# Kernel optimization log

Measured on AMD Instinct MI355X. Metric: run time of the kernel, lower is better.

The kernel has to match this reference:

```python
import jax, jax.numpy as jnp
import numpy as np

DIM = 1024
HEADS = 16
HEAD_DIM = DIM // HEADS


def setup_inputs() -> dict:
    key = jax.random.key(0)
    ks = jax.random.split(key, 9)
    s = 1.0 / np.sqrt(DIM)
    return {
        "x": jax.random.normal(ks[0], (2, 2048, 1, DIM), dtype=jnp.float32),
        "Wq": jax.random.normal(ks[1], (DIM, DIM), dtype=jnp.float32) * s,
        "bq": jnp.zeros((DIM,), dtype=jnp.float32),
        "Wk": jax.random.normal(ks[2], (DIM, DIM), dtype=jnp.float32) * s,
        "bk": jnp.zeros((DIM,), dtype=jnp.float32),
        "Wv": jax.random.normal(ks[3], (DIM, DIM), dtype=jnp.float32) * s,
        "bv": jnp.zeros((DIM,), dtype=jnp.float32),
        "Wo": jax.random.normal(ks[4], (DIM, DIM), dtype=jnp.float32) * s,
        "bo": jnp.zeros((DIM,), dtype=jnp.float32),
    }


def reference(x, Wq, bq, Wk, bk, Wv, bv, Wo, bo):
    b, t, _, d = x.shape
    h, hd = HEADS, HEAD_DIM
    # torch Linear: y = x @ W.T + b
    q = (x @ Wq.T + bq).reshape(b, t, h, hd)
    k = (x @ Wk.T + bk).reshape(b, t, h, hd)
    v = (x @ Wv.T + bv).reshape(b, t, h, hd)
    # Source applies self.scaling (hd**-0.5) in torch AND divides by
    # sqrt(k_features) inside the jax chunk routine -> net scale 1/hd.
    q = q * (1.0 / hd)
    # key_chunk_size >= T -> one chunk; online softmax == exact stable softmax
    scores = jnp.einsum('bqhd,bkhd->bhqk', q, k)  # [B,H,T,T]
    w = jax.nn.softmax(scores, axis=-1)
    o = jnp.einsum('bhqk,bkhd->bqhd', w, v).reshape(b, t, d)
    return o @ Wo.T + bo
```

## Files before the change

### kernel.cpp

```cpp
#include <hip/hip_runtime.h>
#include <math.h>

typedef _Float16 f16;
typedef _Float16 f16x2 __attribute__((ext_vector_type(2)));
typedef _Float16 f16x4 __attribute__((ext_vector_type(4)));
typedef _Float16 f16x8 __attribute__((ext_vector_type(8)));
typedef float    f32x4 __attribute__((ext_vector_type(4)));

constexpr int DIM   = 1024;
constexpr int HEADS = 16;
constexpr int HD    = 64;
constexpr int BATCH = 2;
constexpr int SEQ   = 2048;
constexpr int MTOT  = BATCH * SEQ;
constexpr int NT2   = SEQ / 128;

#define QSCALE (1.4426950408889634f / 64.0f)

#define MFMA16(a, b, c) __builtin_amdgcn_mfma_f32_16x16x32_f16((a), (b), (c), 0, 0, 0)

__device__ __forceinline__ void glds16(const void* g, void* l) {
    __builtin_amdgcn_global_load_lds(
        (const __attribute__((address_space(1))) void*)g,
        (__attribute__((address_space(3))) void*)l, 16, 0, 0);
}

__device__ __forceinline__ float exp2_hw(float x) {
    float r;
    asm("v_exp_f32 %0, %1" : "=v"(r) : "v"(x));
    return r;
}

__device__ __forceinline__ f16x2 pk_f16(float a, float b) {
    return __builtin_bit_cast(f16x2, __builtin_amdgcn_cvt_pkrtz(a, b));
}

__global__ __launch_bounds__(256) void presplit_kernel(
    const float* __restrict__ x,  const float* __restrict__ Wq,
    const float* __restrict__ Wk, const float* __restrict__ Wv,
    const float* __restrict__ Wo,
    f16* __restrict__ Xh,  f16* __restrict__ WqH, f16* __restrict__ WkH,
    f16* __restrict__ WvH, f16* __restrict__ WoH)
{
    const int bid = blockIdx.x;
    const float* src; f16* dh; int row;
    if (bid < 4096)      { src = x;  dh = Xh;  row = bid; }
    else if (bid < 5120) { src = Wq; dh = WqH; row = bid - 4096; }
    else if (bid < 6144) { src = Wk; dh = WkH; row = bid - 5120; }
    else if (bid < 7168) { src = Wv; dh = WvH; row = bid - 6144; }
    else                 { src = Wo; dh = WoH; row = bid - 7168; }

    const int k = threadIdx.x * 4;
    const float4 v = *reinterpret_cast<const float4*>(&src[(size_t)row * DIM + k]);
    const int s = (row >> 1) & 3;
    const size_t o = (size_t)row * DIM + (k & ~31) + ((k & 31) ^ (s << 3));
    f16x4 h4;
    h4[0] = (f16)v.x; h4[1] = (f16)v.y; h4[2] = (f16)v.z; h4[3] = (f16)v.w;
    *reinterpret_cast<f16x4*>(&dh[o]) = h4;
}

template <int MODE>
__device__ __forceinline__ void gemm_plane_body(
    const f16* __restrict__ AhG, const f16* __restrict__ BhG,
    const float* __restrict__ bias, float* __restrict__ C,
    f16* __restrict__ F, float scale, f16* __restrict__ smem)
{
    f16* Ah = smem;
    f16* Bh = smem + 8192;

    const int tid = threadIdx.x;
    const int l   = tid & 63;
    const int w   = tid >> 6;
    const int wm  = (w >> 1) * 64;
    const int wn  = (w & 1) * 64;
    const int m0  = blockIdx.y * 128;
    const int n0  = blockIdx.x * 128;
    const int fr  = l & 15;
    const int fk  = (l >> 4) * 8;
    const int rg  = (l >> 4) * 4;
    const int fko = fk ^ (((fr >> 1) & 3) << 3);

    f32x4 acc[4][4] = {};

    for (int k0 = 0; k0 < DIM; k0 += 64) {
        __syncthreads();
        #pragma unroll
        for (int j = 0; j < 8; ++j) {
            const int c  = w * 8 + j;
            const int p  = c >> 4;
            const int cc = c & 15;
            const f16* P = (p == 0) ? AhG : BhG;
            const int r0 = (p == 0) ? m0 : n0;
            const int row = r0 + cc * 8 + (l >> 3);
            glds16(P + (size_t)row * DIM + k0 + (l & 7) * 8, smem + c * 512);
        }
        asm volatile("s_waitcnt vmcnt(0)" ::: "memory");
        __syncthreads();

        f16x8 ah[2][4], bh[2][4];
        #pragma unroll
        for (int ks = 0; ks < 2; ++ks) {
            #pragma unroll
            for (int m = 0; m < 4; ++m)
                ah[ks][m] = *reinterpret_cast<const f16x8*>(
                    &Ah[(wm + m * 16 + fr) * 64 + ks * 32 + fko]);
            #pragma unroll
            for (int n = 0; n < 4; ++n)
                bh[ks][n] = *reinterpret_cast<const f16x8*>(
                    &Bh[(wn + n * 16 + fr) * 64 + ks * 32 + fko]);
        }
        #pragma unroll
        for (int ks = 0; ks < 2; ++ks)
            #pragma unroll
            for (int n = 0; n < 4; ++n)
                #pragma unroll
                for (int m = 0; m < 4; ++m) {
                    if (MODE == 1)
                        acc[m][n] = MFMA16(bh[ks][n], ah[ks][m], acc[m][n]);
                    else
                        acc[m][n] = MFMA16(ah[ks][m], bh[ks][n], acc[m][n]);
                }
    }

    if (MODE == 0 || MODE == 3) {
        #pragma unroll
        for (int n = 0; n < 4; ++n) {
            const int col  = n0 + wn + n * 16 + fr;
            const float bb = bias[col];
            #pragma unroll
            for (int m = 0; m < 4; ++m) {
                #pragma unroll
                for (int r = 0; r < 4; ++r) {
                    const int row = m0 + wm + m * 16 + rg + r;
                    const float v = (acc[m][n][r] + bb) * scale;
                    if (MODE == 0) C[(size_t)row * DIM + col] = v;
                    else           F[(size_t)row * DIM + col] = (f16)v;
                }
            }
        }
    } else if (MODE == 1) {
        constexpr int RS = 72;
        const int batch = m0 >> 11;
        const int kvg0  = m0 & 2047;
        for (int s = 0; s < 2; ++s) {
            __syncthreads();
            if ((w & 1) == s) {
                #pragma unroll
                for (int n = 0; n < 4; ++n) {
                    #pragma unroll
                    for (int m = 0; m < 4; ++m) {
                        const int kvrow = wm + m * 16 + fr;
                        const int dd    = n * 16 + rg;
                        f16x4 h4;
                        #pragma unroll
                        for (int r = 0; r < 4; ++r)
                            h4[r] = (f16)(acc[m][n][r] + bias[n0 + wn + dd + r]);
                        const int o = kvrow * RS + (dd ^ ((kvrow & 7) << 3));
                        *reinterpret_cast<f16x4*>(&smem[o]) = h4;
                    }
                }
            }
            __syncthreads();
            const size_t bh_ = (size_t)batch * HEADS + (n0 >> 6) + s;
            const int row = tid >> 1, c0 = (tid & 1) * 32;
            #pragma unroll
            for (int j = 0; j < 4; ++j) {
                const int so = row * RS + c0 + j * 8;
                const size_t go = bh_ * 131072 + (size_t)(kvg0 + row) * 64 + c0 + j * 8;
                *reinterpret_cast<f16x8*>(&F[go]) =
                    *reinterpret_cast<const f16x8*>(&smem[so]);
            }
        }
    } else {
        constexpr int RS = 136;
        const int batch = m0 >> 11;
        const int kvg0  = m0 & 2047;
        for (int s = 0; s < 2; ++s) {
            __syncthreads();
            if ((w & 1) == s) {
                #pragma unroll
                for (int n = 0; n < 4; ++n) {
                    const int d    = n * 16 + fr;
                    const float bb = bias[n0 + wn + d];
                    #pragma unroll
                    for (int m = 0; m < 4; ++m) {
                        const int kvl = wm + m * 16 + rg;
                        f16x4 h4;
                        h4[0] = (f16)(acc[m][n][0] + bb);
                        h4[1] = (f16)(acc[m][n][1] + bb);
                        h4[2] = (f16)(acc[m][n][2] + bb);
                        h4[3] = (f16)(acc[m][n][3] + bb);
                        const int o = d * RS + (kvl ^ ((d & 7) << 3));
                        *reinterpret_cast<f16x4*>(&smem[o]) = h4;
                    }
                }
            }
            __syncthreads();
            const size_t bh_ = (size_t)batch * HEADS + (n0 >> 6) + s;
            const int row = tid >> 2, c0 = (tid & 3) * 32;
            #pragma unroll
            for (int j = 0; j < 4; ++j) {
                const int so = row * RS + c0 + j * 8;
                const size_t go = bh_ * 131072 + (size_t)row * 2048 + kvg0 + c0 + j * 8;
                *reinterpret_cast<f16x8*>(&F[go]) =
                    *reinterpret_cast<const f16x8*>(&smem[so]);
            }
        }
    }
}

__global__ __launch_bounds__(256) void qkv_kernel(
    const f16* __restrict__ XhG,
    const f16* __restrict__ WqH, const float* __restrict__ bq,
    const f16* __restrict__ WkH, const float* __restrict__ bk,
    const f16* __restrict__ WvH, const float* __restrict__ bv,
    f16* __restrict__ QhG, f16* __restrict__ KhG, f16* __restrict__ VhG)
{
    __shared__ __align__(16) f16 smem[18432];
    if (blockIdx.z == 0)
        gemm_plane_body<3>(XhG, WqH, bq, nullptr, QhG, QSCALE, smem);
    else if (blockIdx.z == 1)
        gemm_plane_body<1>(XhG, WkH, bk, nullptr, KhG, 1.0f, smem);
    else
        gemm_plane_body<2>(XhG, WvH, bv, nullptr, VhG, 1.0f, smem);
}

__global__ __launch_bounds__(256) void oproj_kernel(
    const f16* __restrict__ OhG, const f16* __restrict__ WoH,
    const float* __restrict__ bo, float* __restrict__ out)
{
    __shared__ __align__(16) f16 smem[16384];
    gemm_plane_body<0>(OhG, WoH, bo, out, nullptr, 1.0f, smem);
}

__global__ __launch_bounds__(256, 2) void attn_kernel(
    const f16* __restrict__ QhG, const f16* __restrict__ KhG,
    const f16* __restrict__ VhG, f16* __restrict__ OhG)
{
    __shared__ __align__(16) f16 lds[2][2][8192];
    __shared__ __align__(16) f16 PL[4][2][1024];

    const int tid = threadIdx.x;
    const int l   = tid & 63;
    const int w   = tid >> 6;
    const int fr  = l & 15;
    const int g   = l >> 4;
    const int fk  = g * 8;
    const int rg  = g * 4;
    const int swz = (fr & 7) << 3;

    const int lin  = blockIdx.x + 16 * (blockIdx.y + 16 * blockIdx.z);
    const int sid  = (lin & 7) * 64 + (lin >> 3);
    const int qblk = sid & 15;
    const int head = (sid >> 4) & 15;
    const int batch = sid >> 8;

    const int q0 = qblk * 128;
    const size_t rowbase = (size_t)batch * SEQ;
    const int hcol = head * HD;
    const size_t bhbase = ((size_t)batch * HEADS + head) * (size_t)(SEQ * HD);

    size_t kA[4], vA[4];
    #pragma unroll
    for (int c = 0; c < 4; ++c) {
        const int h0 = (w * 4 + c) * 512 + l * 8;
        kA[c] = bhbase + (size_t)h0;
        vA[c] = bhbase + (size_t)(h0 >> 7) * 2048 + (h0 & 127);
    }

#define STAGE(B, T) do {                                                    \
        const size_t _ko = (size_t)(T) * 8192;                              \
        const size_t _vo = (size_t)(T) * 128;                               \
        _Pragma("unroll")                                                   \
        for (int c = 0; c < 4; ++c) {                                       \
            const int lo_ = (w * 4 + c) * 512;                              \
            glds16(KhG + kA[c] + _ko, &lds[B][0][lo_]);                     \
            glds16(VhG + vA[c] + _vo, &lds[B][1][lo_]);                     \
        }                                                                   \
    } while (0)

    STAGE(0, 0);

    f16x8 qh[2][2];
    #pragma unroll
    for (int qb = 0; qb < 2; ++qb) {
        const f16* qp = &QhG[(rowbase + q0 + w * 32 + qb * 16 + fr) * DIM + hcol];
        qh[qb][0] = *reinterpret_cast<const f16x8*>(&qp[fk]);
        qh[qb][1] = *reinterpret_cast<const f16x8*>(&qp[32 + fk]);
    }

    f16x8 onesv;
    #pragma unroll
    for (int i = 0; i < 8; ++i) onesv[i] = (f16)1.0f;

    f32x4 ls[2] = {};
    f32x4 oa[4][2] = {};

    int cur = 0;
    for (int t = 0; t < NT2; ++t) {
        asm volatile("s_waitcnt vmcnt(0) lgkmcnt(0)\ns_barrier" ::: "memory");
        if (t + 1 < NT2) STAGE(cur ^ 1, t + 1);

        #pragma unroll
        for (int hh = 0; hh < 2; ++hh) {
            const f16* Kh = &lds[cur][0][hh * 4096];
            const f16* Vh = &lds[cur][1][hh * 64];

            f32x4 sa[4][2] = {};
            __builtin_amdgcn_s_setprio(1);
            #pragma unroll
            for (int kvb = 0; kvb < 4; ++kvb) {
                #pragma unroll
                for (int ks = 0; ks < 2; ++ks) {
                    const int o = ((kvb * 16 + fr) * 64 + ks * 32 + fk) ^ swz;
                    const f16x8 kh = *reinterpret_cast<const f16x8*>(&Kh[o]);
                    sa[kvb][0] = MFMA16(kh, qh[0][ks], sa[kvb][0]);
                    sa[kvb][1] = MFMA16(kh, qh[1][ks], sa[kvb][1]);
                }
            }
            __builtin_amdgcn_s_setprio(0);

            f16x8 pf[2][2];
            #pragma unroll
            for (int qb = 0; qb < 2; ++qb) {
                f16* Wh = &PL[w][qb][0];
                #pragma unroll
                for (int kvb = 0; kvb < 4; ++kvb) {
                    const f16x2 p01 = pk_f16(exp2_hw(sa[kvb][qb][0]),
                                             exp2_hw(sa[kvb][qb][1]));
                    const f16x2 p23 = pk_f16(exp2_hw(sa[kvb][qb][2]),
                                             exp2_hw(sa[kvb][qb][3]));
                    f16x4 h4;
                    h4[0] = p01[0]; h4[1] = p01[1]; h4[2] = p23[0]; h4[3] = p23[1];
                    const int po = (fr * 64 + kvb * 16 + rg) ^ swz;
                    *reinterpret_cast<f16x4*>(&Wh[po]) = h4;
                }
                #pragma unroll
                for (int ks = 0; ks < 2; ++ks) {
                    const int ro = (fr * 64 + ks * 32 + fk) ^ swz;
                    pf[qb][ks] = *reinterpret_cast<const f16x8*>(&Wh[ro]);
                }
            }

            __builtin_amdgcn_s_setprio(1);
            #pragma unroll
            for (int qb = 0; qb < 2; ++qb)
                #pragma unroll
                for (int ks = 0; ks < 2; ++ks)
                    ls[qb] = MFMA16(onesv, pf[qb][ks], ls[qb]);
            #pragma unroll
            for (int db = 0; db < 4; ++db) {
                #pragma unroll
                for (int ks = 0; ks < 2; ++ks) {
                    const int vo = (db * 16 + fr) * 128 + ((ks * 32 + fk) ^ swz);
                    const f16x8 vh = *reinterpret_cast<const f16x8*>(&Vh[vo]);
                    oa[db][0] = MFMA16(vh, pf[0][ks], oa[db][0]);
                    oa[db][1] = MFMA16(vh, pf[1][ks], oa[db][1]);
                }
            }
            __builtin_amdgcn_s_setprio(0);
        }
        cur ^= 1;
    }
#undef STAGE

    #pragma unroll
    for (int qb = 0; qb < 2; ++qb) {
        const float inv = 1.0f / ls[qb][0];
        const size_t row = rowbase + q0 + w * 32 + qb * 16 + fr;
        const int s = ((int)row >> 1) & 3;
        #pragma unroll
        for (int db = 0; db < 4; ++db) {
            f16x4 h4;
            #pragma unroll
            for (int j = 0; j < 4; ++j) h4[j] = (f16)(oa[db][qb][j] * inv);
            const int kg = hcol + db * 16 + rg;
            const size_t o = row * DIM + (kg & ~31) + ((kg & 31) ^ (s << 3));
            *reinterpret_cast<f16x4*>(&OhG[o]) = h4;
        }
    }
}

extern "C" void kernel_launch(void* const* d_in, const int* in_sizes, int n_in,
                              void* d_out, int out_size, void* d_ws, size_t ws_size,
                              hipStream_t stream)
{
    const float* x  = (const float*)d_in[0];
    const float* Wq = (const float*)d_in[1];
    const float* bq = (const float*)d_in[2];
    const float* Wk = (const float*)d_in[3];
    const float* bk = (const float*)d_in[4];
    const float* Wv = (const float*)d_in[5];
    const float* bv = (const float*)d_in[6];
    const float* Wo = (const float*)d_in[7];
    const float* bo = (const float*)d_in[8];
    float* out = (float*)d_out;

    const size_t PS = (size_t)MTOT * DIM;
    f16* QhG = (f16*)d_ws;
    f16* KhG = QhG + PS;
    f16* VhG = KhG + PS;
    f16* XhG = VhG + PS;
    f16* WqH = XhG + PS;
    f16* WkH = WqH + (size_t)DIM * DIM;
    f16* WvH = WkH + (size_t)DIM * DIM;
    f16* WoH = WvH + (size_t)DIM * DIM;
    f16* OhG = XhG;

    presplit_kernel<<<8192, 256, 0, stream>>>(x, Wq, Wk, Wv, Wo,
                                              XhG, WqH, WkH, WvH, WoH);

    dim3 gqkv(DIM / 128, MTOT / 128, 3);
    qkv_kernel<<<gqkv, 256, 0, stream>>>(XhG, WqH, bq, WkH, bk, WvH, bv,
                                         QhG, KhG, VhG);

    dim3 gattn(SEQ / 128, HEADS, BATCH);
    attn_kernel<<<gattn, 256, 0, stream>>>(QhG, KhG, VhG, OhG);

    dim3 gout(DIM / 128, MTOT / 128);
    oproj_kernel<<<gout, 256, 0, stream>>>(OhG, WoH, bo, out);
}
```

Before: 124.7 us.

## Double-buffer GEMM LDS tiles with K-step 32 and prefetch overlap

Replaces the single-buffered K=64 tile loop in the projection GEMM with a double-buffered K=32 loop. The next tile is issued via global_load_lds while the current one feeds MFMAs, and partial vmcnt waits plus raw barriers stand in for __syncthreads. This is meant to hide global load latency behind compute, at the cost of twice as many loop iterations and barriers. The swizzle (fko) is kept from the 64-wide layout while the row stride is now 32, which risks bank conflicts or a layout mismatch.

```diff
diff --git a/kernel.cpp b/kernel.cpp
--- a/kernel.cpp
+++ b/kernel.cpp
@@ -65,9 +65,6 @@
     const float* __restrict__ bias, float* __restrict__ C,
     f16* __restrict__ F, float scale, f16* __restrict__ smem)
 {
-    f16* Ah = smem;
-    f16* Bh = smem + 8192;
-
     const int tid = threadIdx.x;
     const int l   = tid & 63;
     const int w   = tid >> 6;
@@ -82,45 +79,53 @@
 
     f32x4 acc[4][4] = {};
 
-    for (int k0 = 0; k0 < DIM; k0 += 64) {
-        __syncthreads();
-        #pragma unroll
-        for (int j = 0; j < 8; ++j) {
-            const int c  = w * 8 + j;
-            const int p  = c >> 4;
-            const int cc = c & 15;
-            const f16* P = (p == 0) ? AhG : BhG;
-            const int r0 = (p == 0) ? m0 : n0;
-            const int row = r0 + cc * 8 + (l >> 3);
-            glds16(P + (size_t)row * DIM + k0 + (l & 7) * 8, smem + c * 512);
-        }
-        asm volatile("s_waitcnt vmcnt(0)" ::: "memory");
-        __syncthreads();
-
-        f16x8 ah[2][4], bh[2][4];
-        #pragma unroll
-        for (int ks = 0; ks < 2; ++ks) {
-            #pragma unroll
-            for (int m = 0; m < 4; ++m)
-                ah[ks][m] = *reinterpret_cast<const f16x8*>(
-                    &Ah[(wm + m * 16 + fr) * 64 + ks * 32 + fko]);
-            #pragma unroll
-            for (int n = 0; n < 4; ++n)
-                bh[ks][n] = *reinterpret_cast<const f16x8*>(
-                    &Bh[(wn + n * 16 + fr) * 64 + ks * 32 + fko]);
-        }
-        #pragma unroll
-        for (int ks = 0; ks < 2; ++ks)
-            #pragma unroll
-            for (int n = 0; n < 4; ++n)
-                #pragma unroll
-                for (int m = 0; m < 4; ++m) {
-                    if (MODE == 1)
-                        acc[m][n] = MFMA16(bh[ks][n], ah[ks][m], acc[m][n]);
-                    else
-                        acc[m][n] = MFMA16(ah[ks][m], bh[ks][n], acc[m][n]);
-                }
-    }
+#define GSTAGE(B, K0) do {                                                  \
+        _Pragma("unroll")                                                   \
+        for (int j = 0; j < 4; ++j) {                                       \
+            const int c = w * 4 + j;                             \
+            const int p = c >> 3;                         \
+            const f16* P = (p == 0) ? AhG : BhG;                            \
+            const int r0 = (p == 0) ? m0 : n0;                              \
+            const int row = r0 + (c & 7) * 16 + (l >> 2);                   \
+            glds16(P + (size_t)row * DIM + (K0) + (l & 3) * 8,              \
+                   smem + (B) * 8192 + c * 512);                            \
+        }                                                                   \
+    } while (0)
+
+    GSTAGE(0, 0);
+    int cur = 0;
+
+    for (int k0 = 0; k0 < DIM; k0 += 32) {
+        if (k0 + 32 < DIM) {
+            GSTAGE(cur ^ 1, k0 + 32);
+            asm volatile("s_waitcnt vmcnt(4)\ns_barrier" ::: "memory");
+        } else {
+            asm volatile("s_waitcnt vmcnt(0)\ns_barrier" ::: "memory");
+        }
+
+        const f16* Ah = smem + cur * 8192;
+        const f16* Bh = Ah + 4096;
+
+        f16x8 ah[4], bh[4];
+        #pragma unroll
+        for (int m = 0; m < 4; ++m)
+            ah[m] = *reinterpret_cast<const f16x8*>(&Ah[(wm + m * 16 + fr) * 32 + fko]);
+        #pragma unroll
+        for (int n = 0; n < 4; ++n)
+            bh[n] = *reinterpret_cast<const f16x8*>(&Bh[(wn + n * 16 + fr) * 32 + fko]);
+        #pragma unroll
+        for (int n = 0; n < 4; ++n)
+            #pragma unroll
+            for (int m = 0; m < 4; ++m) {
+                if (MODE == 1)
+                    acc[m][n] = MFMA16(bh[n], ah[m], acc[m][n]);
+                else
+                    acc[m][n] = MFMA16(ah[m], bh[n], acc[m][n]);
+            }
+        asm volatile("s_barrier" ::: "memory");
+        cur ^= 1;
+    }
+#undef GSTAGE
 
     if (MODE == 0 || MODE == 3) {
         #pragma unroll
```

Result: faster. 115.9 us (-7.0%).
